# Optimization experiments

Hardware: AMD Instinct MI355X
Metric: run time of the kernel (lower is better)

Reference implementation:

```python
import jax, jax.numpy as jnp
import numpy as np

B, T, N, F_OUT, K, HID = 8, 12, 4096, 12, 3, 64
HALF = T // 2


def setup_inputs() -> dict:
    key = jax.random.key(0)
    ks = jax.random.split(key, 7)
    return {
        "x": jax.random.normal(ks[0], (B, T, N, 1), jnp.float32),
        "adj": jax.random.normal(ks[1], (K, N, N), jnp.float32) / np.float32(np.sqrt(N)),
        "cheb_w": jax.random.normal(ks[2], (HID, K), jnp.float32) / np.float32(np.sqrt(K)),
        "gcn_w": jax.random.normal(ks[3], (F_OUT, T, 1, HID), jnp.float32) / np.float32(np.sqrt(T * HID)),
        "gcn_b": jnp.zeros((F_OUT,), jnp.float32),
        "glu1_w": jax.random.normal(ks[4], (F_OUT, HALF, 3, 3), jnp.float32) / np.float32(np.sqrt(HALF * 9)),
        "glu1_b": jnp.zeros((F_OUT,), jnp.float32),
        "glu2_w": jax.random.normal(ks[5], (F_OUT, HALF, 3, 3), jnp.float32) / np.float32(np.sqrt(HALF * 9)),
        "glu2_b": jnp.zeros((F_OUT,), jnp.float32),
    }


def _dilated_conv(x, w, b):
    # Conv2d(kernel=3, dilation=2, padding=2) on (B, C, N, 1)
    y = jax.lax.conv_general_dilated(
        x, w, window_strides=(1, 1), padding=((2, 2), (2, 2)),
        rhs_dilation=(2, 2), dimension_numbers=("NCHW", "OIHW", "NCHW"))
    return y + b[None, :, None, None]


def reference(x, adj, cheb_w, gcn_w, gcn_b, glu1_w, glu1_b, glu2_w, glu2_b):
    # --- ChebConv (vectorized over the per-channel Python loop) ---
    # x: (B, T, N, 1), adj: (K, N, N) -> y: (B, T, N, K)
    y = jnp.einsum("knm,btm->btnk", adj, x[..., 0])
    # Linear(K -> HID, no bias) + ReLU -> cheb: (B, T, N, HID)
    cheb = jax.nn.relu(jnp.einsum("btnk,ok->btno", y, cheb_w))
    # --- gcn_conv: Conv2d(T -> F_OUT, kernel (1, HID)) -> (B, F_OUT, N, 1) ---
    sgc = jnp.einsum("btnj,otj->bon", cheb, gcn_w[:, :, 0, :]) + gcn_b[None, :, None]
    sgc = sgc[..., None]
    # --- GLU path: split history in half, dilated convs, a * sigmoid(g) ---
    x_u, x_v = x[:, :HALF], x[:, HALF:]
    a = _dilated_conv(x_u, glu1_w, glu1_b)
    g = _dilated_conv(x_v, glu2_w, glu2_b)
    x_glu = a * jax.nn.sigmoid(g)
    return x_glu + sgc
```

## Files before the change

### kernel.cpp

```cpp
#include <hip/hip_runtime.h>
#include <hip/hip_bf16.h>
#include <math.h>

#define NNODES 4096
#define NCOLS  96
#define NROWS  12288
#define KSEG   4
#define KLEN   (NNODES / KSEG)
#define BKS    64
#define NSTEP  (KLEN / BKS)
#define BMR    48

typedef __attribute__((ext_vector_type(8))) short short8;
typedef __attribute__((ext_vector_type(4))) float float4v;

__global__ void probe_dtype(const unsigned int* __restrict__ aw, int* __restrict__ flag) {
    int tid = threadIdx.x;
    unsigned w = aw[tid];
    unsigned e = (w >> 7) & 0xffu;
    bool insane = (e >= 0xC0u) || (e <= 0x30u);
    unsigned long long m = __ballot(insane);
    if (tid == 0) flag[0] = (__popcll(m) >= 16) ? 1 : 0;
}

__device__ __forceinline__ float ldf(const void* p, size_t i, int isf32) {
    return isf32 ? ((const float*)p)[i]
                 : __bfloat162float(((const __hip_bfloat16*)p)[i]);
}

__device__ __forceinline__ void ld8(float* d, const void* p, size_t e, int isf32) {
    if (isf32) {
        const float4* s = (const float4*)((const float*)p + e);
        float4 f0 = s[0], f1 = s[1];
        d[0] = f0.x; d[1] = f0.y; d[2] = f0.z; d[3] = f0.w;
        d[4] = f1.x; d[5] = f1.y; d[6] = f1.z; d[7] = f1.w;
    } else {
        const __hip_bfloat16* s = (const __hip_bfloat16*)p + e;
#pragma unroll
        for (int j = 0; j < 8; j++) d[j] = __bfloat162float(s[j]);
    }
}

__device__ __forceinline__ short8 cvt8(float4 a, float4 b) {
    union { short8 v; __hip_bfloat16 h[8]; } u;
    u.h[0] = __float2bfloat16(a.x); u.h[1] = __float2bfloat16(a.y);
    u.h[2] = __float2bfloat16(a.z); u.h[3] = __float2bfloat16(a.w);
    u.h[4] = __float2bfloat16(b.x); u.h[5] = __float2bfloat16(b.y);
    u.h[6] = __float2bfloat16(b.z); u.h[7] = __float2bfloat16(b.w);
    return u.v;
}

__global__ __launch_bounds__(256) void cvt_x(
    const void* __restrict__ xv, __hip_bfloat16* __restrict__ xbf,
    const int* __restrict__ flag)
{
    const int isf32 = flag[0];
    const int i = (blockIdx.x * 256 + threadIdx.x) * 8;
    if (isf32) {
        const float* xf = (const float*)xv;
        float4 f0 = *(const float4*)(xf + i);
        float4 f1 = *(const float4*)(xf + i + 4);
        short8 v = cvt8(f0, f1);
        *(short8*)(xbf + i) = v;
    } else {
        *(uint4*)(xbf + i) = *(const uint4*)((const __hip_bfloat16*)xv + i);
    }
}

__global__ __launch_bounds__(192, 3) void gemm_y(
    const void* __restrict__ adjv, const __hip_bfloat16* __restrict__ xbf,
    float* __restrict__ yws, const int* __restrict__ flag)
{
    __shared__ uint4 Xs[3][96 * 8];

    const int tid = threadIdx.x;
    const int isf32 = flag[0];
    const int wv = tid >> 6, ln = tid & 63, fr = ln & 15, fq = ln >> 4;

    const int bid = blockIdx.x;
    const int rt0 = (bid >> 2) * BMR;
    const int ks  = bid & 3;
    const int k0  = ks * KLEN;

    float4v acc[6];
#pragma unroll
    for (int i = 0; i < 6; i++) acc[i] = (float4v){0.f, 0.f, 0.f, 0.f};

    int xslot_[4];
    const __hip_bfloat16* xsrc[4];
#pragma unroll
    for (int s = 0; s < 4; s++) {
        int L = s * 192 + tid;
        int r = L >> 3, c = L & 7;
        xslot_[s] = r * 8 + (c ^ (r & 7));
        xsrc[s] = xbf + (size_t)r * NNODES + k0 + c * 8;
    }

    const int arow = rt0 + wv * 16 + fr;

#define XLOAD(R, STEP) { _Pragma("unroll")                                     \
    for (int s = 0; s < 4; s++) R[s] = *(const uint4*)(xsrc[s] + (size_t)(STEP) * BKS); }
#define XWRITE(R, BUF) { _Pragma("unroll")                                     \
    for (int s = 0; s < 4; s++) Xs[BUF][xslot_[s]] = R[s]; }
#define BARRIER() { asm volatile("s_waitcnt lgkmcnt(0)" ::: "memory");         \
    __builtin_amdgcn_s_barrier();                                              \
    __builtin_amdgcn_sched_barrier(0); }

    if (isf32) {
        const float* ap = (const float*)adjv + (size_t)arow * NNODES + k0 + fq * 8;
        uint4 XA[4], XB[4];
        float4 AA[2][2], AB[2][2];

#define ALOADF(R, STEP) { _Pragma("unroll")                                    \
        for (int kq = 0; kq < 2; kq++) {                                       \
            const float* p = ap + (STEP) * BKS + kq * 32;                      \
            R[kq][0] = *(const float4*)p; R[kq][1] = *(const float4*)(p + 4); } }
#define COMPF(R, BUF) { _Pragma("unroll")                                      \
        for (int kq = 0; kq < 2; kq++) {                                       \
            short8 a = cvt8(R[kq][0], R[kq][1]);                               \
            _Pragma("unroll")                                                  \
            for (int ct = 0; ct < 6; ct++) {                                   \
                short8 b = *(const short8*)&Xs[BUF][(ct * 16 + fr) * 8 +       \
                                                    ((kq * 4 + fq) ^ (fr & 7))]; \
                acc[ct] = __builtin_amdgcn_mfma_f32_16x16x32_bf16(a, b, acc[ct], 0, 0, 0); \
            } } }

        XLOAD(XA, 0); ALOADF(AA, 0);
        XLOAD(XB, 1); ALOADF(AB, 1);
        XWRITE(XA, 0);
        BARRIER();

        int b0 = 0;
        for (int t = 0; t < NSTEP; t += 2) {
            if (t + 1 < NSTEP) XWRITE(XB, (b0 + 1) % 3);
            if (t + 2 < NSTEP) XLOAD(XA, t + 2);
            COMPF(AA, b0);
            if (t + 2 < NSTEP) ALOADF(AA, t + 2);
            BARRIER();
            if (t + 2 < NSTEP) XWRITE(XA, (b0 + 2) % 3);
            if (t + 3 < NSTEP) XLOAD(XB, t + 3);
            COMPF(AB, (b0 + 1) % 3);
            if (t + 3 < NSTEP) ALOADF(AB, t + 3);
            BARRIER();
            b0 = (b0 + 2) % 3;
        }
#undef ALOADF
#undef COMPF
    } else {
        const __hip_bfloat16* ap = (const __hip_bfloat16*)adjv + (size_t)arow * NNODES + k0 + fq * 8;
        uint4 XA[4], XB[4];
        uint4 AA[2], AB[2];

#define ALOADB(R, STEP) { _Pragma("unroll")                                    \
        for (int kq = 0; kq < 2; kq++)                                         \
            R[kq] = *(const uint4*)(ap + (STEP) * BKS + kq * 32); }
#define COMPB(R, BUF) { _Pragma("unroll")                                      \
        for (int kq = 0; kq < 2; kq++) {                                       \
            short8 a = *(const short8*)&R[kq];                                 \
            _Pragma("unroll")                                                  \
            for (int ct = 0; ct < 6; ct++) {                                   \
                short8 b = *(const short8*)&Xs[BUF][(ct * 16 + fr) * 8 +       \
                                                    ((kq * 4 + fq) ^ (fr & 7))]; \
                acc[ct] = __builtin_amdgcn_mfma_f32_16x16x32_bf16(a, b, acc[ct], 0, 0, 0); \
            } } }

        XLOAD(XA, 0); ALOADB(AA, 0);
        XLOAD(XB, 1); ALOADB(AB, 1);
        XWRITE(XA, 0);
        BARRIER();

        int b0 = 0;
        for (int t = 0; t < NSTEP; t += 2) {
            if (t + 1 < NSTEP) XWRITE(XB, (b0 + 1) % 3);
            if (t + 2 < NSTEP) XLOAD(XA, t + 2);
            COMPB(AA, b0);
            if (t + 2 < NSTEP) ALOADB(AA, t + 2);
            BARRIER();
            if (t + 2 < NSTEP) XWRITE(XA, (b0 + 2) % 3);
            if (t + 3 < NSTEP) XLOAD(XB, t + 3);
            COMPB(AB, (b0 + 1) % 3);
            if (t + 3 < NSTEP) ALOADB(AB, t + 3);
            BARRIER();
            b0 = (b0 + 2) % 3;
        }
#undef ALOADB
#undef COMPB
    }
#undef XLOAD
#undef XWRITE
#undef BARRIER

    float* yo = yws + (size_t)ks * NROWS * NCOLS;
#pragma unroll
    for (int ct = 0; ct < 6; ct++)
#pragma unroll
        for (int rg = 0; rg < 4; rg++) {
            size_t r = (size_t)rt0 + wv * 16 + fq * 4 + rg;
            yo[r * NCOLS + ct * 16 + fr] = acc[ct][rg];
        }
}

__global__ __launch_bounds__(256) void epilogue_kernel(
    const void* __restrict__ xv, const float* __restrict__ yws,
    const void* __restrict__ chebv, const void* __restrict__ gcnwv,
    const void* __restrict__ gcnbv, const void* __restrict__ g1wv,
    const void* __restrict__ g1bv, const void* __restrict__ g2wv,
    const void* __restrict__ g2bv,
    float* __restrict__ out, const int* __restrict__ flag)
{
    __shared__ float gwL[9216];
    __shared__ float cwL[192];
    __shared__ float w1L[216];
    __shared__ float w2L[216];
    __shared__ float wbL[36];

    const int tid = threadIdx.x;
    const int isf32 = flag[0];

    for (int i = tid; i < 9216; i += 256) {
        int o = i / 768, t = (i / 64) % 12, j = i % 64;
        gwL[t * 768 + j * 12 + o] = ldf(gcnwv, i, isf32);
    }
    if (tid < 192) cwL[tid] = ldf(chebv, tid, isf32);
    if (tid < 216) {
        w1L[tid] = ldf(g1wv, (size_t)tid * 3 + 1, isf32);
        w2L[tid] = ldf(g2wv, (size_t)tid * 3 + 1, isf32);
    }
    if (tid < 12) {
        wbL[tid]      = ldf(gcnbv, tid, isf32);
        wbL[12 + tid] = ldf(g1bv, tid, isf32);
        wbL[24 + tid] = ldf(g2bv, tid, isf32);
    }
    __syncthreads();

    const int gid = blockIdx.x * 256 + tid;
    const int pr  = gid >> 2;
    const int tq  = gid & 3;
    const int b = pr >> 12;
    const int n = pr & (NNODES - 1);

    float yk[3][3];
#pragma unroll
    for (int k = 0; k < 3; k++) { yk[k][0] = 0.f; yk[k][1] = 0.f; yk[k][2] = 0.f; }
#pragma unroll
    for (int s = 0; s < KSEG; s++) {
        const float* base = yws + (size_t)s * NROWS * NCOLS;
#pragma unroll
        for (int k = 0; k < 3; k++) {
            const float* yp = base + ((size_t)(k * NNODES + n)) * NCOLS + b * 12 + tq * 3;
            yk[k][0] += yp[0]; yk[k][1] += yp[1]; yk[k][2] += yp[2];
        }
    }

    float sg[12];
#pragma unroll
    for (int o = 0; o < 12; o++) sg[o] = 0.f;
#pragma unroll
    for (int i = 0; i < 3; i++) {
        const float y0 = yk[0][i], y1 = yk[1][i], y2 = yk[2][i];
        const float* gwt = gwL + (tq * 3 + i) * 768;
#pragma unroll 4
        for (int j = 0; j < 64; j++) {
            float h = y0 * cwL[j * 3] + y1 * cwL[j * 3 + 1] + y2 * cwL[j * 3 + 2];
            h = fmaxf(h, 0.f);
#pragma unroll
            for (int o = 0; o < 12; o++) sg[o] += h * gwt[j * 12 + o];
        }
    }
#pragma unroll
    for (int o = 0; o < 12; o++) {
        sg[o] += __shfl_xor(sg[o], 1);
        sg[o] += __shfl_xor(sg[o], 2);
    }

    float xa[18], xg[18];
#pragma unroll
    for (int c = 0; c < 6; c++)
#pragma unroll
        for (int kh = 0; kh < 3; kh++) {
            int m = n + 2 * kh - 2;
            bool ok = ((unsigned)m < (unsigned)NNODES);
            xa[c * 3 + kh] = ok ? ldf(xv, ((size_t)(b * 12 + c)) * NNODES + m, isf32) : 0.f;
            xg[c * 3 + kh] = ok ? ldf(xv, ((size_t)(b * 12 + c + 6)) * NNODES + m, isf32) : 0.f;
        }

#pragma unroll
    for (int i = 0; i < 3; i++) {
        const int o = tq * 3 + i;
        float av = wbL[12 + o], gv = wbL[24 + o];
#pragma unroll
        for (int q = 0; q < 18; q++) {
            av += xa[q] * w1L[o * 18 + q];
            gv += xg[q] * w2L[o * 18 + q];
        }
        float s = 1.f / (1.f + expf(-gv));
        out[((size_t)(b * 12 + o)) * NNODES + n] = av * s + sg[o] + wbL[o];
    }
}

__global__ __launch_bounds__(64) void fused_simple(
    const void* __restrict__ xv, const void* __restrict__ adjv,
    const void* __restrict__ chebv, const void* __restrict__ gcnwv,
    const void* __restrict__ gcnbv, const void* __restrict__ g1wv,
    const void* __restrict__ g1bv, const void* __restrict__ g2wv,
    const void* __restrict__ g2bv,
    float* __restrict__ out, const int* __restrict__ flag)
{
    __shared__ float gwL[9216];
    __shared__ float cwL[192];
    __shared__ float w1L[216];
    __shared__ float w2L[216];
    __shared__ float wbL[36];

    const int tid = threadIdx.x;
    const int isf32 = flag[0];

    for (int i = tid; i < 9216; i += 64) {
        int o = i / 768, t = (i / 64) % 12, j = i % 64;
        gwL[t * 768 + j * 12 + o] = ldf(gcnwv, i, isf32);
    }
    for (int i = tid; i < 192; i += 64) cwL[i] = ldf(chebv, i, isf32);
    for (int i = tid; i < 216; i += 64) {
        w1L[i] = ldf(g1wv, (size_t)i * 3 + 1, isf32);
        w2L[i] = ldf(g2wv, (size_t)i * 3 + 1, isf32);
    }
    if (tid < 12) {
        wbL[tid]      = ldf(gcnbv, tid, isf32);
        wbL[12 + tid] = ldf(g1bv, tid, isf32);
        wbL[24 + tid] = ldf(g2bv, tid, isf32);
    }
    __syncthreads();

    const int g = blockIdx.x * 64 + tid;
    const int b = g >> 12;
    const int n = g & (NNODES - 1);

    float y[3][12];
#pragma unroll
    for (int k = 0; k < 3; k++)
#pragma unroll
        for (int t = 0; t < 12; t++) y[k][t] = 0.f;

    for (int m0 = 0; m0 < NNODES; m0 += 8) {
        float a0[8], a1[8], a2[8];
        ld8(a0, adjv, ((size_t)(0 * NNODES + n)) * NNODES + m0, isf32);
        ld8(a1, adjv, ((size_t)(1 * NNODES + n)) * NNODES + m0, isf32);
        ld8(a2, adjv, ((size_t)(2 * NNODES + n)) * NNODES + m0, isf32);
#pragma unroll
        for (int t = 0; t < 12; t++) {
            float x8[8];
            ld8(x8, xv, ((size_t)(b * 12 + t)) * NNODES + m0, isf32);
#pragma unroll
            for (int j = 0; j < 8; j++) {
                y[0][t] += a0[j] * x8[j];
                y[1][t] += a1[j] * x8[j];
                y[2][t] += a2[j] * x8[j];
            }
        }
    }

    float sg[12];
#pragma unroll
    for (int o = 0; o < 12; o++) sg[o] = wbL[o];
    for (int t = 0; t < 12; t++) {
        const float y0 = y[0][t], y1 = y[1][t], y2 = y[2][t];
        const float* gwt = gwL + t * 768;
#pragma unroll 4
        for (int j = 0; j < 64; j++) {
            float h = y0 * cwL[j * 3] + y1 * cwL[j * 3 + 1] + y2 * cwL[j * 3 + 2];
            h = fmaxf(h, 0.f);
#pragma unroll
            for (int o = 0; o < 12; o++) sg[o] += h * gwt[j * 12 + o];
        }
    }

    float xa[18], xg[18];
#pragma unroll
    for (int c = 0; c < 6; c++)
#pragma unroll
        for (int kh = 0; kh < 3; kh++) {
            int m = n + 2 * kh - 2;
            bool ok = ((unsigned)m < (unsigned)NNODES);
            xa[c * 3 + kh] = ok ? ldf(xv, ((size_t)(b * 12 + c)) * NNODES + m, isf32) : 0.f;
            xg[c * 3 + kh] = ok ? ldf(xv, ((size_t)(b * 12 + c + 6)) * NNODES + m, isf32) : 0.f;
        }

#pragma unroll
    for (int o = 0; o < 12; o++) {
        float av = wbL[12 + o], gv = wbL[24 + o];
#pragma unroll
        for (int i = 0; i < 18; i++) {
            av += xa[i] * w1L[o * 18 + i];
            gv += xg[i] * w2L[o * 18 + i];
        }
        float s = 1.f / (1.f + expf(-gv));
        out[((size_t)(b * 12 + o)) * NNODES + n] = av * s + sg[o];
    }
}

extern "C" void kernel_launch(void* const* d_in, const int* in_sizes, int n_in,
                              void* d_out, int out_size, void* d_ws, size_t ws_size,
                              hipStream_t stream)
{
    int* flag = (int*)d_ws;
    __hip_bfloat16* xbf = (__hip_bfloat16*)((char*)d_ws + 64);
    float* yws = (float*)((char*)d_ws + 64 + (size_t)NCOLS * NNODES * 2);
    const size_t need = 64 + (size_t)NCOLS * NNODES * 2
                      + (size_t)KSEG * NROWS * NCOLS * 4;

    hipLaunchKernelGGL(probe_dtype, dim3(1), dim3(64), 0, stream,
                       (const unsigned int*)d_in[1], flag);

    if (ws_size >= need) {
        hipLaunchKernelGGL(cvt_x, dim3(192), dim3(256), 0, stream,
                           d_in[0], xbf, flag);
        hipLaunchKernelGGL(gemm_y, dim3(256 * KSEG), dim3(192), 0, stream,
                           d_in[1], xbf, yws, flag);
        hipLaunchKernelGGL(epilogue_kernel, dim3(512), dim3(256), 0, stream,
                           d_in[0], yws, d_in[2], d_in[3], d_in[4],
                           d_in[5], d_in[6], d_in[7], d_in[8],
                           (float*)d_out, flag);
    } else {
        hipLaunchKernelGGL(fused_simple, dim3(512), dim3(64), 0, stream,
                           d_in[0], d_in[1], d_in[2], d_in[3], d_in[4],
                           d_in[5], d_in[6], d_in[7], d_in[8],
                           (float*)d_out, flag);
    }
}
```

Before: 422.3 us.

## Raise split-K to 16 and stage the whole X slice in LDS once

The adjacency GEMM now splits K into 16 segments instead of 4, with 512-thread blocks covering 128 rows each. Each block loads its entire 96x256 bf16 X slice into LDS once, so the triple-buffered X pipeline and its per-step barriers go away, and only the A loads are double-buffered in registers. The aim is more parallelism and less synchronisation in a GEMM that streams a large adjacency matrix. The cost is a partial-sum workspace four times larger, which adds write and read traffic in the epilogue. If the workspace is too small, execution drops to the slow fallback kernel.

Measured after the change: 375.9 us. -11.0%, faster.

```diff
diff --git a/kernel.cpp b/kernel.cpp
--- a/kernel.cpp
+++ b/kernel.cpp
@@ -5,11 +5,9 @@
 #define NNODES 4096
 #define NCOLS  96
 #define NROWS  12288
-#define KSEG   4
+#define KSEG   16
 #define KLEN   (NNODES / KSEG)
-#define BKS    64
-#define NSTEP  (KLEN / BKS)
-#define BMR    48
+#define NST    (KLEN / 32)
 
 typedef __attribute__((ext_vector_type(8))) short short8;
 typedef __attribute__((ext_vector_type(4))) float float4v;
@@ -67,128 +65,84 @@
     }
 }
 
-__global__ __launch_bounds__(192, 3) void gemm_y(
+__global__ __launch_bounds__(512, 4) void gemm_y(
     const void* __restrict__ adjv, const __hip_bfloat16* __restrict__ xbf,
     float* __restrict__ yws, const int* __restrict__ flag)
 {
-    __shared__ uint4 Xs[3][96 * 8];
+    __shared__ uint4 Xs[96 * 32];
 
     const int tid = threadIdx.x;
     const int isf32 = flag[0];
     const int wv = tid >> 6, ln = tid & 63, fr = ln & 15, fq = ln >> 4;
 
     const int bid = blockIdx.x;
-    const int rt0 = (bid >> 2) * BMR;
-    const int ks  = bid & 3;
+    const int rt0 = (bid >> 4) * 128;
+    const int ks  = bid & 15;
     const int k0  = ks * KLEN;
 
+#pragma unroll
+    for (int s = 0; s < 6; s++) {
+        int L = tid + s * 512;
+        int r = L >> 5, c = L & 31;
+        Xs[r * 32 + (c ^ (r & 7))] =
+            *(const uint4*)(xbf + (size_t)r * NNODES + k0 + c * 8);
+    }
+
     float4v acc[6];
 #pragma unroll
     for (int i = 0; i < 6; i++) acc[i] = (float4v){0.f, 0.f, 0.f, 0.f};
 
-    int xslot_[4];
-    const __hip_bfloat16* xsrc[4];
-#pragma unroll
-    for (int s = 0; s < 4; s++) {
-        int L = s * 192 + tid;
-        int r = L >> 3, c = L & 7;
-        xslot_[s] = r * 8 + (c ^ (r & 7));
-        xsrc[s] = xbf + (size_t)r * NNODES + k0 + c * 8;
-    }
-
     const int arow = rt0 + wv * 16 + fr;
-
-#define XLOAD(R, STEP) { _Pragma("unroll")                                     \
-    for (int s = 0; s < 4; s++) R[s] = *(const uint4*)(xsrc[s] + (size_t)(STEP) * BKS); }
-#define XWRITE(R, BUF) { _Pragma("unroll")                                     \
-    for (int s = 0; s < 4; s++) Xs[BUF][xslot_[s]] = R[s]; }
-#define BARRIER() { asm volatile("s_waitcnt lgkmcnt(0)" ::: "memory");         \
-    __builtin_amdgcn_s_barrier();                                              \
-    __builtin_amdgcn_sched_barrier(0); }
+    __syncthreads();
+
+#define XFRAG(CT, STEP) \
+    (*(const short8*)&Xs[((CT) * 16 + fr) * 32 + ((((STEP) * 4) + fq) ^ (((CT) * 16 + fr) & 7))])
 
     if (isf32) {
         const float* ap = (const float*)adjv + (size_t)arow * NNODES + k0 + fq * 8;
-        uint4 XA[4], XB[4];
-        float4 AA[2][2], AB[2][2];
-
-#define ALOADF(R, STEP) { _Pragma("unroll")                                    \
-        for (int kq = 0; kq < 2; kq++) {                                       \
-            const float* p = ap + (STEP) * BKS + kq * 32;                      \
-            R[kq][0] = *(const float4*)p; R[kq][1] = *(const float4*)(p + 4); } }
-#define COMPF(R, BUF) { _Pragma("unroll")                                      \
-        for (int kq = 0; kq < 2; kq++) {                                       \
-            short8 a = cvt8(R[kq][0], R[kq][1]);                               \
-            _Pragma("unroll")                                                  \
-            for (int ct = 0; ct < 6; ct++) {                                   \
-                short8 b = *(const short8*)&Xs[BUF][(ct * 16 + fr) * 8 +       \
-                                                    ((kq * 4 + fq) ^ (fr & 7))]; \
-                acc[ct] = __builtin_amdgcn_mfma_f32_16x16x32_bf16(a, b, acc[ct], 0, 0, 0); \
-            } } }
-
-        XLOAD(XA, 0); ALOADF(AA, 0);
-        XLOAD(XB, 1); ALOADF(AB, 1);
-        XWRITE(XA, 0);
-        BARRIER();
-
-        int b0 = 0;
-        for (int t = 0; t < NSTEP; t += 2) {
-            if (t + 1 < NSTEP) XWRITE(XB, (b0 + 1) % 3);
-            if (t + 2 < NSTEP) XLOAD(XA, t + 2);
-            COMPF(AA, b0);
-            if (t + 2 < NSTEP) ALOADF(AA, t + 2);
-            BARRIER();
-            if (t + 2 < NSTEP) XWRITE(XA, (b0 + 2) % 3);
-            if (t + 3 < NSTEP) XLOAD(XB, t + 3);
-            COMPF(AB, (b0 + 1) % 3);
-            if (t + 3 < NSTEP) ALOADF(AB, t + 3);
-            BARRIER();
-            b0 = (b0 + 2) % 3;
-        }
+        float4 AA[2], AB[2];
+
+#define ALOADF(R, STEP) { const float* p = ap + (STEP) * 32;                   \
+        R[0] = *(const float4*)p; R[1] = *(const float4*)(p + 4); }
+#define COMPF(R, STEP) { short8 a = cvt8(R[0], R[1]);                          \
+        _Pragma("unroll")                                                      \
+        for (int ct = 0; ct < 6; ct++)                                         \
+            acc[ct] = __builtin_amdgcn_mfma_f32_16x16x32_bf16(a, XFRAG(ct, STEP), acc[ct], 0, 0, 0); }
+
+        ALOADF(AA, 0); ALOADF(AB, 1);
+        COMPF(AA, 0);  ALOADF(AA, 2);
+        COMPF(AB, 1);  ALOADF(AB, 3);
+        COMPF(AA, 2);  ALOADF(AA, 4);
+        COMPF(AB, 3);  ALOADF(AB, 5);
+        COMPF(AA, 4);  ALOADF(AA, 6);
+        COMPF(AB, 5);  ALOADF(AB, 7);
+        COMPF(AA, 6);
+        COMPF(AB, 7);
 #undef ALOADF
 #undef COMPF
     } else {
         const __hip_bfloat16* ap = (const __hip_bfloat16*)adjv + (size_t)arow * NNODES + k0 + fq * 8;
-        uint4 XA[4], XB[4];
-        uint4 AA[2], AB[2];
-
-#define ALOADB(R, STEP) { _Pragma("unroll")                                    \
-        for (int kq = 0; kq < 2; kq++)                                         \
-            R[kq] = *(const uint4*)(ap + (STEP) * BKS + kq * 32); }
-#define COMPB(R, BUF) { _Pragma("unroll")                                      \
-        for (int kq = 0; kq < 2; kq++) {                                       \
-            short8 a = *(const short8*)&R[kq];                                 \
-            _Pragma("unroll")                                                  \
-            for (int ct = 0; ct < 6; ct++) {                                   \
-                short8 b = *(const short8*)&Xs[BUF][(ct * 16 + fr) * 8 +       \
-                                                    ((kq * 4 + fq) ^ (fr & 7))]; \
-                acc[ct] = __builtin_amdgcn_mfma_f32_16x16x32_bf16(a, b, acc[ct], 0, 0, 0); \
-            } } }
-
-        XLOAD(XA, 0); ALOADB(AA, 0);
-        XLOAD(XB, 1); ALOADB(AB, 1);
-        XWRITE(XA, 0);
-        BARRIER();
-
-        int b0 = 0;
-        for (int t = 0; t < NSTEP; t += 2) {
-            if (t + 1 < NSTEP) XWRITE(XB, (b0 + 1) % 3);
-            if (t + 2 < NSTEP) XLOAD(XA, t + 2);
-            COMPB(AA, b0);
-            if (t + 2 < NSTEP) ALOADB(AA, t + 2);
-            BARRIER();
-            if (t + 2 < NSTEP) XWRITE(XA, (b0 + 2) % 3);
-            if (t + 3 < NSTEP) XLOAD(XB, t + 3);
-            COMPB(AB, (b0 + 1) % 3);
-            if (t + 3 < NSTEP) ALOADB(AB, t + 3);
-            BARRIER();
-            b0 = (b0 + 2) % 3;
-        }
+        uint4 AA, AB;
+
+#define ALOADB(R, STEP) R = *(const uint4*)(ap + (STEP) * 32);
+#define COMPB(R, STEP) { short8 a = *(const short8*)&R;                        \
+        _Pragma("unroll")                                                      \
+        for (int ct = 0; ct < 6; ct++)                                         \
+            acc[ct] = __builtin_amdgcn_mfma_f32_16x16x32_bf16(a, XFRAG(ct, STEP), acc[ct], 0, 0, 0); }
+
+        ALOADB(AA, 0); ALOADB(AB, 1);
+        COMPB(AA, 0);  ALOADB(AA, 2);
+        COMPB(AB, 1);  ALOADB(AB, 3);
+        COMPB(AA, 2);  ALOADB(AA, 4);
+        COMPB(AB, 3);  ALOADB(AB, 5);
+        COMPB(AA, 4);  ALOADB(AA, 6);
+        COMPB(AB, 5);  ALOADB(AB, 7);
+        COMPB(AA, 6);
+        COMPB(AB, 7);
 #undef ALOADB
 #undef COMPB
     }
-#undef XLOAD
-#undef XWRITE
-#undef BARRIER
+#undef XFRAG
 
     float* yo = yws + (size_t)ks * NROWS * NCOLS;
 #pragma unroll
@@ -242,7 +196,7 @@
     float yk[3][3];
 #pragma unroll
     for (int k = 0; k < 3; k++) { yk[k][0] = 0.f; yk[k][1] = 0.f; yk[k][2] = 0.f; }
-#pragma unroll
+#pragma unroll 4
     for (int s = 0; s < KSEG; s++) {
         const float* base = yws + (size_t)s * NROWS * NCOLS;
 #pragma unroll
@@ -414,7 +368,7 @@
     if (ws_size >= need) {
         hipLaunchKernelGGL(cvt_x, dim3(192), dim3(256), 0, stream,
                            d_in[0], xbf, flag);
-        hipLaunchKernelGGL(gemm_y, dim3(256 * KSEG), dim3(192), 0, stream,
+        hipLaunchKernelGGL(gemm_y, dim3(96 * KSEG), dim3(512), 0, stream,
                            d_in[1], xbf, yws, flag);
         hipLaunchKernelGGL(epilogue_kernel, dim3(512), dim3(256), 0, stream,
                            d_in[0], yws, d_in[2], d_in[3], d_in[4],
```
